# Kernel optimization log

Measured on AMD Instinct MI355X. Metric: run time of the kernel, lower is better.

## Reference

```python
import jax, jax.numpy as jnp
import numpy as np

DOWNSCALE = 2

def setup_inputs() -> dict:
    key = jax.random.key(0)
    k1, k2, k3 = jax.random.split(key, 3)
    B, C, H, W = 8, 128, 256, 256
    Cr = C // 4
    fm = jax.random.normal(k1, (B, C, H, W), dtype=jnp.float32)
    # torch Linear weight is [out,in]; store transposed [in,out] for x @ W
    Wq = jax.random.normal(k2, (C, Cr), dtype=jnp.float32) * (1.0 / np.sqrt(C))
    Wk = jax.random.normal(k3, (C, Cr), dtype=jnp.float32) * (1.0 / np.sqrt(C))
    return {"fm": fm, "Wq": Wq, "Wk": Wk}

def reference(fm, Wq, Wk):
    d = DOWNSCALE
    B, C, H, W = fm.shape
    nH, nW = H // d, W // d
    # [B,C,H,W] -> [B,nH,nW,d*d,C] windows
    x = fm.reshape(B, C, nH, d, nW, d)
    x = jnp.transpose(x, (0, 2, 4, 3, 5, 1)).reshape(B, nH, nW, d * d, C)
    # mean query over window tokens
    q = jnp.mean(x, axis=-2)                      # [B,nH,nW,C]
    q = (q @ Wq) * (Wq.shape[-1] ** -0.5)         # [B,nH,nW,Cr]
    k = x @ Wk                                    # [B,nH,nW,d*d,Cr]
    qk = jnp.einsum('bhwr,bhwtr->bhwt', q, k)     # [B,nH,nW,d*d]
    attn = jax.nn.softmax(qk, axis=-1)
    out = jnp.einsum('bhwt,bhwtc->bhwc', attn, x) # [B,nH,nW,C]
    return jnp.transpose(out, (0, 3, 1, 2))       # [B,C,nH,nW]
```

## Files before the change

### kernel.cpp

```cpp
#include <hip/hip_runtime.h>

#define BB   8
#define CCH  128
#define CR   32
#define HH   256
#define WW   256
#define NHH  128
#define NWW  128

#define WPB  16
#define TPB  128
#define TS   65
#define QMS  20
#define GS   17

__global__ void compute_m_kernel(const float* __restrict__ Wq,
                                 const float* __restrict__ Wk,
                                 float* __restrict__ M) {
    int idx = blockIdx.x * blockDim.x + threadIdx.x;
    int cp = idx >> 7;
    int c  = idx & 127;
    float s = 0.f;
#pragma unroll
    for (int r = 0; r < CR; ++r)
        s += Wq[cp * CR + r] * Wk[c * CR + r];
    M[idx] = s * 0.17677669529663687f;
}

__global__ __launch_bounds__(TPB)
void attn_downsample_kernel(const float* __restrict__ fm,
                            const float* __restrict__ M,
                            float* __restrict__ out) {
    __shared__ float tile[CCH][TS];
    __shared__ float qm[CCH][QMS];
    __shared__ float gl[CCH][GS];
    __shared__ float attn_t[4][WPB];

    const int wseg = blockIdx.x;
    const int nh   = blockIdx.y;
    const int b    = blockIdx.z;
    const int t    = threadIdx.x;

    const int w0   = wseg * (WPB * 2);
    const int row0 = nh * 2;

#pragma unroll 4
    for (int k = 0; k < 16; ++k) {
        int q  = k * TPB + t;
        int c  = q >> 4;
        int rj = (q & 15) << 2;
        int r  = rj >> 5;
        int j  = rj & 31;
        const float4 v = *reinterpret_cast<const float4*>(
            fm + (((b * CCH + c) * HH + row0 + r) * WW + w0 + j));
        tile[c][rj + 0] = v.x;
        tile[c][rj + 1] = v.y;
        tile[c][rj + 2] = v.z;
        tile[c][rj + 3] = v.w;
    }
    __syncthreads();

    {
        int jw = t & 15;
        int cg = t >> 4;
#pragma unroll 4
        for (int i = 0; i < 16; ++i) {
            int c = cg * 16 + i;
            float s = tile[c][2 * jw] + tile[c][2 * jw + 1]
                    + tile[c][32 + 2 * jw] + tile[c][32 + 2 * jw + 1];
            qm[c][jw] = 0.25f * s;
        }
    }
    __syncthreads();

    {
        int c = t;
        float g[16];
#pragma unroll
        for (int k = 0; k < 16; ++k) g[k] = 0.f;

#pragma unroll 4
        for (int cp = 0; cp < 128; ++cp) {
            float m = M[cp * 128 + c];
            const float4 a0 = *reinterpret_cast<const float4*>(&qm[cp][0]);
            const float4 a1 = *reinterpret_cast<const float4*>(&qm[cp][4]);
            const float4 a2 = *reinterpret_cast<const float4*>(&qm[cp][8]);
            const float4 a3 = *reinterpret_cast<const float4*>(&qm[cp][12]);
            g[0]  += a0.x * m;  g[1]  += a0.y * m;  g[2]  += a0.z * m;  g[3]  += a0.w * m;
            g[4]  += a1.x * m;  g[5]  += a1.y * m;  g[6]  += a1.z * m;  g[7]  += a1.w * m;
            g[8]  += a2.x * m;  g[9]  += a2.y * m;  g[10] += a2.z * m;  g[11] += a2.w * m;
            g[12] += a3.x * m;  g[13] += a3.y * m;  g[14] += a3.z * m;  g[15] += a3.w * m;
        }
#pragma unroll
        for (int k = 0; k < 16; ++k) gl[c][k] = g[k];
    }
    __syncthreads();

    {
        int jw   = t >> 3;
        int tsub = t & 7;
        float qk0 = 0.f, qk1 = 0.f, qk2 = 0.f, qk3 = 0.f;
#pragma unroll 4
        for (int i = 0; i < 16; ++i) {
            int c = tsub * 16 + i;
            float g  = gl[c][jw];
            qk0 += g * tile[c][2 * jw];
            qk1 += g * tile[c][2 * jw + 1];
            qk2 += g * tile[c][32 + 2 * jw];
            qk3 += g * tile[c][32 + 2 * jw + 1];
        }
#pragma unroll
        for (int off = 1; off < 8; off <<= 1) {
            qk0 += __shfl_xor(qk0, off);
            qk1 += __shfl_xor(qk1, off);
            qk2 += __shfl_xor(qk2, off);
            qk3 += __shfl_xor(qk3, off);
        }
        float mx = fmaxf(fmaxf(qk0, qk1), fmaxf(qk2, qk3));
        float e0 = expf(qk0 - mx);
        float e1 = expf(qk1 - mx);
        float e2 = expf(qk2 - mx);
        float e3 = expf(qk3 - mx);
        float inv = 1.0f / (e0 + e1 + e2 + e3);
        if (tsub == 0) {
            attn_t[0][jw] = e0 * inv;
            attn_t[1][jw] = e1 * inv;
            attn_t[2][jw] = e2 * inv;
            attn_t[3][jw] = e3 * inv;
        }
    }
    __syncthreads();

    {
        int jw = t & 15;
        int cg = t >> 4;
        float a0 = attn_t[0][jw];
        float a1 = attn_t[1][jw];
        float a2 = attn_t[2][jw];
        float a3 = attn_t[3][jw];
        int ow = wseg * WPB + jw;
#pragma unroll 4
        for (int i = 0; i < 16; ++i) {
            int c = cg * 16 + i;
            float o = a0 * tile[c][2 * jw]
                    + a1 * tile[c][2 * jw + 1]
                    + a2 * tile[c][32 + 2 * jw]
                    + a3 * tile[c][32 + 2 * jw + 1];
            out[((b * CCH + c) * NHH + nh) * NWW + ow] = o;
        }
    }
}

extern "C" void kernel_launch(void* const* d_in, const int* in_sizes, int n_in,
                              void* d_out, int out_size, void* d_ws, size_t ws_size,
                              hipStream_t stream) {
    const float* fm = (const float*)d_in[0];
    const float* Wq = (const float*)d_in[1];
    const float* Wk = (const float*)d_in[2];
    float* outp = (float*)d_out;
    float* Mws  = (float*)d_ws;

    compute_m_kernel<<<dim3(64), dim3(256), 0, stream>>>(Wq, Wk, Mws);

    dim3 grid(NWW / WPB, NHH, BB);
    attn_downsample_kernel<<<grid, dim3(TPB), 0, stream>>>(fm, Mws, outp);
}
```

Measured before the change: 486.8 us.

## Halve window tile per block and register-block the query-key projection GEMM

Each block now covers 8 output windows instead of 16, doubling the grid and cutting shared memory per block. The M-times-query product is register-blocked as 4 channels by 8 windows per thread with float4 loads of M, and partial sums across channel groups are reduced with DPP adds. The per-channel tile reads, the pooled query and the output stores are vectorized as float4, and the fast __expf is used in the softmax. In exchange, the smaller blocks mean more blocks reload M and redo fixed setup, and the output store now writes 8 contiguous floats per channel.

```diff
diff --git a/kernel.cpp b/kernel.cpp
--- a/kernel.cpp
+++ b/kernel.cpp
@@ -2,17 +2,15 @@
 
 #define BB   8
 #define CCH  128
-#define CR   32
 #define HH   256
 #define WW   256
 #define NHH  128
 #define NWW  128
 
-#define WPB  16
+#define WPB  8
 #define TPB  128
-#define TS   65
-#define QMS  20
-#define GS   17
+#define TS   36
+#define QS   8
 
 __global__ void compute_m_kernel(const float* __restrict__ Wq,
                                  const float* __restrict__ Wk,
@@ -22,132 +20,161 @@
     int c  = idx & 127;
     float s = 0.f;
 #pragma unroll
-    for (int r = 0; r < CR; ++r)
-        s += Wq[cp * CR + r] * Wk[c * CR + r];
+    for (int r = 0; r < 32; ++r)
+        s += Wq[cp * 32 + r] * Wk[c * 32 + r];
     M[idx] = s * 0.17677669529663687f;
 }
 
+template <int CTRL>
+__device__ __forceinline__ float dpp_add(float v) {
+    int x = __builtin_amdgcn_update_dpp(0, __float_as_int(v), CTRL, 0xF, 0xF, true);
+    return v + __int_as_float(x);
+}
+
 __global__ __launch_bounds__(TPB)
-void attn_downsample_kernel(const float* __restrict__ fm,
-                            const float* __restrict__ M,
-                            float* __restrict__ out) {
+void attn_ds2(const float* __restrict__ fm, const float* __restrict__ M,
+              float* __restrict__ out) {
     __shared__ float tile[CCH][TS];
-    __shared__ float qm[CCH][QMS];
-    __shared__ float gl[CCH][GS];
-    __shared__ float attn_t[4][WPB];
+    __shared__ float qg[CCH][QS];
+    __shared__ float4 attn4[WPB];
 
     const int wseg = blockIdx.x;
     const int nh   = blockIdx.y;
     const int b    = blockIdx.z;
     const int t    = threadIdx.x;
 
-    const int w0   = wseg * (WPB * 2);
+    const int w0   = wseg * 16;
     const int row0 = nh * 2;
 
-#pragma unroll 4
-    for (int k = 0; k < 16; ++k) {
-        int q  = k * TPB + t;
-        int c  = q >> 4;
-        int rj = (q & 15) << 2;
-        int r  = rj >> 5;
-        int j  = rj & 31;
+#pragma unroll
+    for (int k = 0; k < 8; ++k) {
+        int q = k * TPB + t;
+        int c = q >> 3;
+        int f = q & 7;
+        int r = f >> 2, j = (f & 3) << 2;
         const float4 v = *reinterpret_cast<const float4*>(
-            fm + (((b * CCH + c) * HH + row0 + r) * WW + w0 + j));
-        tile[c][rj + 0] = v.x;
-        tile[c][rj + 1] = v.y;
-        tile[c][rj + 2] = v.z;
-        tile[c][rj + 3] = v.w;
+            fm + (((size_t)(b * CCH + c) * HH + row0 + r) * WW + w0 + j));
+        *reinterpret_cast<float4*>(&tile[c][r * 16 + j]) = v;
     }
     __syncthreads();
 
     {
-        int jw = t & 15;
-        int cg = t >> 4;
-#pragma unroll 4
-        for (int i = 0; i < 16; ++i) {
-            int c = cg * 16 + i;
-            float s = tile[c][2 * jw] + tile[c][2 * jw + 1]
-                    + tile[c][32 + 2 * jw] + tile[c][32 + 2 * jw + 1];
-            qm[c][jw] = 0.25f * s;
+        float p[32];
+#pragma unroll
+        for (int k = 0; k < 8; ++k)
+            *reinterpret_cast<float4*>(&p[k * 4]) =
+                *reinterpret_cast<const float4*>(&tile[t][k * 4]);
+        float qa[4], qb[4];
+#pragma unroll
+        for (int w = 0; w < 4; ++w)
+            qa[w] = 0.25f * (p[2*w] + p[2*w+1] + p[16+2*w] + p[16+2*w+1]);
+#pragma unroll
+        for (int w = 0; w < 4; ++w) {
+            int ww = w + 4;
+            qb[w] = 0.25f * (p[2*ww] + p[2*ww+1] + p[16+2*ww] + p[16+2*ww+1]);
         }
+        *reinterpret_cast<float4*>(&qg[t][0]) = make_float4(qa[0], qa[1], qa[2], qa[3]);
+        *reinterpret_cast<float4*>(&qg[t][4]) = make_float4(qb[0], qb[1], qb[2], qb[3]);
     }
     __syncthreads();
 
     {
-        int c = t;
-        float g[16];
+        const int l   = t & 63;
+        const int wv  = t >> 6;
+        const int cpg = l & 3;
+        const int cg  = l >> 2;
+        const int c0  = wv * 64 + cg * 4;
+
+        float acc[4][8];
 #pragma unroll
-        for (int k = 0; k < 16; ++k) g[k] = 0.f;
+        for (int i = 0; i < 4; ++i)
+#pragma unroll
+            for (int w = 0; w < 8; ++w) acc[i][w] = 0.f;
 
 #pragma unroll 4
-        for (int cp = 0; cp < 128; ++cp) {
-            float m = M[cp * 128 + c];
-            const float4 a0 = *reinterpret_cast<const float4*>(&qm[cp][0]);
-            const float4 a1 = *reinterpret_cast<const float4*>(&qm[cp][4]);
-            const float4 a2 = *reinterpret_cast<const float4*>(&qm[cp][8]);
-            const float4 a3 = *reinterpret_cast<const float4*>(&qm[cp][12]);
-            g[0]  += a0.x * m;  g[1]  += a0.y * m;  g[2]  += a0.z * m;  g[3]  += a0.w * m;
-            g[4]  += a1.x * m;  g[5]  += a1.y * m;  g[6]  += a1.z * m;  g[7]  += a1.w * m;
-            g[8]  += a2.x * m;  g[9]  += a2.y * m;  g[10] += a2.z * m;  g[11] += a2.w * m;
-            g[12] += a3.x * m;  g[13] += a3.y * m;  g[14] += a3.z * m;  g[15] += a3.w * m;
+        for (int k = 0; k < 32; ++k) {
+            int cp = 4 * k + cpg;
+            const float4 m4 = *reinterpret_cast<const float4*>(M + cp * 128 + c0);
+            const float4 qa = *reinterpret_cast<const float4*>(&qg[cp][0]);
+            const float4 qb = *reinterpret_cast<const float4*>(&qg[cp][4]);
+            const float mm[4] = {m4.x, m4.y, m4.z, m4.w};
+            const float qq[8] = {qa.x, qa.y, qa.z, qa.w, qb.x, qb.y, qb.z, qb.w};
+#pragma unroll
+            for (int i = 0; i < 4; ++i)
+#pragma unroll
+                for (int w = 0; w < 8; ++w)
+                    acc[i][w] += mm[i] * qq[w];
         }
+
 #pragma unroll
-        for (int k = 0; k < 16; ++k) gl[c][k] = g[k];
+        for (int i = 0; i < 4; ++i)
+#pragma unroll
+            for (int w = 0; w < 8; ++w) {
+                acc[i][w] = dpp_add<0xB1>(acc[i][w]);
+                acc[i][w] = dpp_add<0x4E>(acc[i][w]);
+            }
+
+        float row[8];
+#pragma unroll
+        for (int w = 0; w < 8; ++w) {
+            float s01 = (cpg & 1) ? acc[1][w] : acc[0][w];
+            float s23 = (cpg & 1) ? acc[3][w] : acc[2][w];
+            row[w] = (cpg & 2) ? s23 : s01;
+        }
+        __syncthreads();
+        *reinterpret_cast<float4*>(&qg[c0 + cpg][0]) =
+            make_float4(row[0], row[1], row[2], row[3]);
+        *reinterpret_cast<float4*>(&qg[c0 + cpg][4]) =
+            make_float4(row[4], row[5], row[6], row[7]);
     }
     __syncthreads();
 
     {
-        int jw   = t >> 3;
-        int tsub = t & 7;
+        const int w = t >> 4;
+        const int tsub = t & 15;
         float qk0 = 0.f, qk1 = 0.f, qk2 = 0.f, qk3 = 0.f;
-#pragma unroll 4
-        for (int i = 0; i < 16; ++i) {
-            int c = tsub * 16 + i;
-            float g  = gl[c][jw];
-            qk0 += g * tile[c][2 * jw];
-            qk1 += g * tile[c][2 * jw + 1];
-            qk2 += g * tile[c][32 + 2 * jw];
-            qk3 += g * tile[c][32 + 2 * jw + 1];
+#pragma unroll
+        for (int i = 0; i < 8; ++i) {
+            int c = i * 16 + tsub;
+            float g = qg[c][w];
+            qk0 += g * tile[c][2 * w];
+            qk1 += g * tile[c][2 * w + 1];
+            qk2 += g * tile[c][16 + 2 * w];
+            qk3 += g * tile[c][16 + 2 * w + 1];
         }
 #pragma unroll
-        for (int off = 1; off < 8; off <<= 1) {
+        for (int off = 1; off < 16; off <<= 1) {
             qk0 += __shfl_xor(qk0, off);
             qk1 += __shfl_xor(qk1, off);
             qk2 += __shfl_xor(qk2, off);
             qk3 += __shfl_xor(qk3, off);
         }
         float mx = fmaxf(fmaxf(qk0, qk1), fmaxf(qk2, qk3));
-        float e0 = expf(qk0 - mx);
-        float e1 = expf(qk1 - mx);
-        float e2 = expf(qk2 - mx);
-        float e3 = expf(qk3 - mx);
+        float e0 = __expf(qk0 - mx);
+        float e1 = __expf(qk1 - mx);
+        float e2 = __expf(qk2 - mx);
+        float e3 = __expf(qk3 - mx);
         float inv = 1.0f / (e0 + e1 + e2 + e3);
-        if (tsub == 0) {
-            attn_t[0][jw] = e0 * inv;
-            attn_t[1][jw] = e1 * inv;
-            attn_t[2][jw] = e2 * inv;
-            attn_t[3][jw] = e3 * inv;
-        }
+        if (tsub == 0)
+            attn4[w] = make_float4(e0 * inv, e1 * inv, e2 * inv, e3 * inv);
     }
     __syncthreads();
 
     {
-        int jw = t & 15;
-        int cg = t >> 4;
-        float a0 = attn_t[0][jw];
-        float a1 = attn_t[1][jw];
-        float a2 = attn_t[2][jw];
-        float a3 = attn_t[3][jw];
-        int ow = wseg * WPB + jw;
-#pragma unroll 4
-        for (int i = 0; i < 16; ++i) {
-            int c = cg * 16 + i;
-            float o = a0 * tile[c][2 * jw]
-                    + a1 * tile[c][2 * jw + 1]
-                    + a2 * tile[c][32 + 2 * jw]
-                    + a3 * tile[c][32 + 2 * jw + 1];
-            out[((b * CCH + c) * NHH + nh) * NWW + ow] = o;
+        float p[32];
+#pragma unroll
+        for (int k = 0; k < 8; ++k)
+            *reinterpret_cast<float4*>(&p[k * 4]) =
+                *reinterpret_cast<const float4*>(&tile[t][k * 4]);
+        float o[8];
+#pragma unroll
+        for (int w = 0; w < 8; ++w) {
+            const float4 a = attn4[w];
+            o[w] = a.x * p[2*w] + a.y * p[2*w+1] + a.z * p[16+2*w] + a.w * p[16+2*w+1];
         }
+        const size_t ob = (((size_t)(b * CCH + t) * NHH + nh) * NWW) + wseg * 8;
+        *reinterpret_cast<float4*>(out + ob)     = make_float4(o[0], o[1], o[2], o[3]);
+        *reinterpret_cast<float4*>(out + ob + 4) = make_float4(o[4], o[5], o[6], o[7]);
     }
 }
 
@@ -163,5 +190,5 @@
     compute_m_kernel<<<dim3(64), dim3(256), 0, stream>>>(Wq, Wk, Mws);
 
     dim3 grid(NWW / WPB, NHH, BB);
-    attn_downsample_kernel<<<grid, dim3(TPB), 0, stream>>>(fm, Mws, outp);
+    attn_ds2<<<grid, dim3(TPB), 0, stream>>>(fm, Mws, outp);
 }
```

Measured after the change: 574.8 us. 18.1% more time.
